# Kernel tuning notes

Hardware: AMD Instinct MI355X
Metric: run time of the kernel (lower is better)

Reference implementation:

```python
import jax, jax.numpy as jnp
import numpy as np

EPS = 1e-08


def setup_inputs() -> dict:
    key = jax.random.key(0)
    k1, k2 = jax.random.split(key)
    n, d = 8192, 64
    x = jax.random.normal(k1, (n, d), dtype=jnp.float32)
    y = jax.random.randint(k2, (n,), 0, 10, dtype=jnp.int64)
    # weights = 1 / temperature_init = 1 / 0.1
    weights = jnp.full((1,), 10.0, dtype=jnp.float32)
    return {"x": x, "y": y, "weights": weights}


def reference(x, y, weights):
    n = x.shape[0]
    # pairwise euclidean distances (torch.cdist p=2)
    sq = jnp.sum(x * x, axis=1)                      # [n]
    d2 = sq[:, None] + sq[None, :] - 2.0 * (x @ x.T)  # [n,n]
    eye = jnp.eye(n, dtype=bool)
    d2 = jnp.maximum(d2, 0.0)
    dist = jnp.where(eye, 0.0, jnp.sqrt(jnp.where(eye, 1.0, d2)))  # safe sqrt on diag
    expo = jnp.exp(-dist * weights[0])               # [n,n]
    same = (y[:, None] == y[None, :]) & ~eye         # same-class, excluding self
    top = jnp.sum(jnp.where(same, expo, 0.0), axis=1)  # [n]
    bot = jnp.sum(jnp.where(~eye, expo, 0.0), axis=1)  # [n]
    fracs = jnp.log(top / (bot + EPS))
    loss = -jnp.mean(fracs)
    return loss
```

## Files before the change

### kernel.cpp

```cpp
#include <hip/hip_runtime.h>

typedef _Float16 f16x8 __attribute__((ext_vector_type(8)));
typedef float    f32x4 __attribute__((ext_vector_type(4)));
typedef float    f32x2 __attribute__((ext_vector_type(2)));

#define N_ROWS 8192
#define DIM 64
#define EPS 1e-8f
#define LOG2E 1.4426950408889634f
#define SHIFT 64.0f
#define SHIFT_LN 44.361419555836499802f
#define TILE_I 256
#define NBI (N_ROWS / TILE_I)
#define TB 512
#define MAXC 17


__global__ void snn_prep(const float* __restrict__ x, _Float16* __restrict__ xh,
                         _Float16* __restrict__ xl, float* __restrict__ sq,
                         float* __restrict__ top, float* __restrict__ bot,
                         float* __restrict__ out) {
    const int gt = blockIdx.x * 256 + threadIdx.x;
    if (gt < N_ROWS) { top[gt] = 0.0f; bot[gt] = 0.0f; }
    if (gt == 0) out[0] = 0.0f;
    const int row = gt >> 6, lane = threadIdx.x & 63;
    float v = x[row * DIM + lane];
    _Float16 h = (_Float16)v;
    _Float16 l = (_Float16)(v - (float)h);
    xh[row * DIM + lane] = h;
    xl[row * DIM + lane] = l;
    float s = v * v;
    #pragma unroll
    for (int off = 32; off > 0; off >>= 1) s += __shfl_xor(s, off, 64);
    if (lane == 0) sq[row] = s;
}

__global__ __launch_bounds__(256, 2) void snn_mfma(
    const _Float16* __restrict__ xh, const _Float16* __restrict__ xl,
    const float* __restrict__ sq, const int* __restrict__ y,
    const float* __restrict__ w,
    float* __restrict__ top, float* __restrict__ bot)
{
    __shared__ float s_sqj[MAXC * 16];
    __shared__ int   s_yj[MAXC * 16];
    __shared__ f32x2 s_j[4][4][MAXC * 16];

    const int bid = blockIdx.x;
    int bi = 0, kk = 0, cum = 0;
    for (int p = 0; p < NBI; p++) {
        int nb = (p < 16) ? p + 1 : p;
        if (bid < cum + nb) { bi = p; kk = bid - cum; break; }
        cum += nb;
    }
    int c0, len;
    if (bi < 16)      { c0 = 16 * kk;              len = 16; }
    else if (kk < 16) { c0 = 17 * kk;              len = 17; }
    else              { c0 = 272 + 16 * (kk - 16); len = 16; }
    const int ndch = min(max(16 * bi - c0, 0), len);
    const int I0 = bi * TILE_I;

    const int tid = threadIdx.x, wv = tid >> 6, lane = tid & 63;
    const int mrow = lane & 15, kq = lane >> 4;

    for (int t = tid; t < len * 16; t += 256) {
        s_sqj[t] = sq[c0 * 16 + t];
        s_yj[t]  = y[c0 * 16 + t];
    }
    __syncthreads();

    const int iw = I0 + wv * 64;

    f16x8 ah[4][2], al[4][2];
    #pragma unroll
    for (int mt = 0; mt < 4; mt++)
        #pragma unroll
        for (int kc = 0; kc < 2; kc++) {
            int a = (iw + mt * 16 + mrow) * DIM + kc * 32 + kq * 8;
            ah[mt][kc] = *(const f16x8*)(xh + a);
            al[mt][kc] = *(const f16x8*)(xl + a);
        }

    float sqi[4][4]; int ypack[4];
    #pragma unroll
    for (int mt = 0; mt < 4; mt++) {
        int yp = 0;
        #pragma unroll
        for (int rr = 0; rr < 4; rr++) {
            int i = iw + mt * 16 + kq * 4 + rr;
            sqi[mt][rr] = sq[i];
            yp |= (y[i] & 255) << (8 * rr);
        }
        ypack[mt] = yp;
    }

    float ts[4][4], bs[4][4];
    #pragma unroll
    for (int mt = 0; mt < 4; mt++)
        #pragma unroll
        for (int rr = 0; rr < 4; rr++) { ts[mt][rr] = 0.0f; bs[mt][rr] = 0.0f; }

    const float c1 = -w[0] * LOG2E;
    f32x4 acc[4];

#define DECL_LOAD(N, NTL)                                                        \
    const int jr##N = (c0 + (NTL)) * 16 + mrow;                                  \
    const int boff##N = jr##N * DIM + kq * 8;                                    \
    f16x8 cbh0##N = *(const f16x8*)(xh + boff##N);                               \
    f16x8 cbh1##N = *(const f16x8*)(xh + boff##N + 32);                          \
    f16x8 cbl0##N = *(const f16x8*)(xl + boff##N);                               \
    f16x8 cbl1##N = *(const f16x8*)(xl + boff##N + 32);                          \
    const float sqj##N = s_sqj[(NTL) * 16 + mrow];                               \
    const int   yj##N  = s_yj[(NTL) * 16 + mrow];

#define DO_MFMA(N)                                                               \
    _Pragma("unroll")                                                            \
    for (int mt = 0; mt < 4; mt++) acc[mt] = (f32x4){0.f, 0.f, 0.f, 0.f};        \
    _Pragma("unroll")                                                            \
    for (int mt = 0; mt < 4; mt++)                                               \
        acc[mt] = __builtin_amdgcn_mfma_f32_16x16x32_f16(ah[mt][0], cbh0##N, acc[mt], 0, 0, 0); \
    _Pragma("unroll")                                                            \
    for (int mt = 0; mt < 4; mt++)                                               \
        acc[mt] = __builtin_amdgcn_mfma_f32_16x16x32_f16(ah[mt][1], cbh1##N, acc[mt], 0, 0, 0); \
    _Pragma("unroll")                                                            \
    for (int mt = 0; mt < 4; mt++)                                               \
        acc[mt] = __builtin_amdgcn_mfma_f32_16x16x32_f16(ah[mt][0], cbl0##N, acc[mt], 0, 0, 0); \
    _Pragma("unroll")                                                            \
    for (int mt = 0; mt < 4; mt++)                                               \
        acc[mt] = __builtin_amdgcn_mfma_f32_16x16x32_f16(ah[mt][1], cbl1##N, acc[mt], 0, 0, 0); \
    _Pragma("unroll")                                                            \
    for (int mt = 0; mt < 4; mt++)                                               \
        acc[mt] = __builtin_amdgcn_mfma_f32_16x16x32_f16(al[mt][0], cbh0##N, acc[mt], 0, 0, 0); \
    _Pragma("unroll")                                                            \
    for (int mt = 0; mt < 4; mt++)                                               \
        acc[mt] = __builtin_amdgcn_mfma_f32_16x16x32_f16(al[mt][1], cbh1##N, acc[mt], 0, 0, 0);

#define EPI_BOTH(N, NTL)                                                         \
    {                                                                            \
        float jt = 0.0f, jb = 0.0f;                                              \
        _Pragma("unroll")                                                        \
        for (int mt = 0; mt < 4; mt++)                                           \
            _Pragma("unroll")                                                    \
            for (int rr = 0; rr < 4; rr++) {                                     \
                float d2 = fmaf(-2.0f, acc[mt][rr], sqi[mt][rr] + sqj##N);       \
                d2 = fmaxf(d2, 0.0f);                                            \
                float dist = __builtin_amdgcn_sqrtf(d2);                         \
                float e2 = __builtin_amdgcn_exp2f(fmaf(c1, dist, SHIFT));        \
                float e2t = (yj##N == ((ypack[mt] >> (8 * rr)) & 255)) ? e2 : 0.0f; \
                ts[mt][rr] += e2t;                                               \
                bs[mt][rr] += e2;                                                \
                jt += e2t;                                                       \
                jb += e2;                                                        \
            }                                                                    \
        s_j[wv][kq][(NTL) * 16 + mrow] = (f32x2){jt, jb};       \
    }

#define EPI_DIAG(N, NTL)                                                         \
    {                                                                            \
        _Pragma("unroll")                                                        \
        for (int mt = 0; mt < 4; mt++)                                           \
            _Pragma("unroll")                                                    \
            for (int rr = 0; rr < 4; rr++) {                                     \
                int i = iw + mt * 16 + kq * 4 + rr;                              \
                float d2 = fmaf(-2.0f, acc[mt][rr], sqi[mt][rr] + sqj##N);       \
                d2 = fmaxf(d2, 0.0f);                                            \
                float dist = __builtin_amdgcn_sqrtf(d2);                         \
                float e2 = __builtin_amdgcn_exp2f(fmaf(c1, dist, SHIFT));        \
                bool offd = (i != jr##N);                                        \
                bool same = offd && (yj##N == ((ypack[mt] >> (8 * rr)) & 255));  \
                bs[mt][rr] += offd ? e2 : 0.0f;                                  \
                ts[mt][rr] += same ? e2 : 0.0f;                                  \
            }                                                                    \
    }

    int ntl = 0;
    for (; ntl + 2 <= ndch; ntl += 2) {
        DECL_LOAD(0, ntl)
        DECL_LOAD(1, ntl + 1)
        DO_MFMA(0) EPI_BOTH(0, ntl)
        DO_MFMA(1) EPI_BOTH(1, ntl + 1)
    }
    for (; ntl < ndch; ntl++) {
        DECL_LOAD(0, ntl)
        DO_MFMA(0) EPI_BOTH(0, ntl)
    }
    for (; ntl + 2 <= len; ntl += 2) {
        DECL_LOAD(0, ntl)
        DECL_LOAD(1, ntl + 1)
        DO_MFMA(0) EPI_DIAG(0, ntl)
        DO_MFMA(1) EPI_DIAG(1, ntl + 1)
    }
    for (; ntl < len; ntl++) {
        DECL_LOAD(0, ntl)
        DO_MFMA(0) EPI_DIAG(0, ntl)
    }
#undef DECL_LOAD
#undef DO_MFMA
#undef EPI_BOTH
#undef EPI_DIAG

    #pragma unroll
    for (int mt = 0; mt < 4; mt++)
        #pragma unroll
        for (int rr = 0; rr < 4; rr++) {
            float tv = ts[mt][rr], bv = bs[mt][rr];
            #pragma unroll
            for (int off = 1; off < 16; off <<= 1) {
                tv += __shfl_xor(tv, off, 64);
                bv += __shfl_xor(bv, off, 64);
            }
            if (mrow == 0) {
                int i = iw + mt * 16 + kq * 4 + rr;
                atomicAdd(&top[i], tv);
                atomicAdd(&bot[i], bv);
            }
        }

    if (ndch > 0) {
        __syncthreads();
        for (int t = tid; t < ndch * 16; t += 256) {
            float tt = 0.0f, bb = 0.0f;
            #pragma unroll
            for (int v = 0; v < 4; v++)
                #pragma unroll
                for (int q = 0; q < 4; q++) {
                    f32x2 s = s_j[v][q][t];
                    tt += s[0];
                    bb += s[1];
                }
            atomicAdd(&top[c0 * 16 + t], tt);
            atomicAdd(&bot[c0 * 16 + t], bb);
        }
    }
}

__global__ __launch_bounds__(256) void snn_final(
    const float* __restrict__ top, const float* __restrict__ bot,
    float* __restrict__ out)
{
    const int i = blockIdx.x * 256 + threadIdx.x;
    float t = top[i];
    float b = bot[i] * 0x1p-64f + EPS;
    float acc = (logf(t) - SHIFT_LN) - logf(b);
    #pragma unroll
    for (int off = 32; off > 0; off >>= 1) acc += __shfl_xor(acc, off, 64);
    __shared__ float red[4];
    if ((threadIdx.x & 63) == 0) red[threadIdx.x >> 6] = acc;
    __syncthreads();
    if (threadIdx.x == 0) {
        float s = red[0] + red[1] + red[2] + red[3];
        atomicAdd(out, -s / (float)N_ROWS);
    }
}

extern "C" void kernel_launch(void* const* d_in, const int* in_sizes, int n_in,
                              void* d_out, int out_size, void* d_ws, size_t ws_size,
                              hipStream_t stream) {
    const float* x = (const float*)d_in[0];
    const int*   y = (const int*)d_in[1];
    const float* w = (const float*)d_in[2];
    float* out = (float*)d_out;

    float* ws  = (float*)d_ws;
    float* top = ws;
    float* bot = ws + N_ROWS;
    float* sq  = ws + 2 * N_ROWS;
    _Float16* xh = (_Float16*)(ws + 3 * N_ROWS);
    _Float16* xl = xh + (size_t)N_ROWS * DIM;

    snn_prep<<<N_ROWS / 4, 256, 0, stream>>>(x, xh, xl, sq, top, bot, out);
    snn_mfma<<<TB, 256, 0, stream>>>(xh, xl, sq, y, w, top, bot);
    snn_final<<<N_ROWS / 256, 256, 0, stream>>>(top, bot, out);
}
```

Baseline: 94.26 us.

## Fuse final reduction into main kernel via last-block counter; vectorize prep

The separate final log/mean kernel is removed. Its work now runs in the last block of the MFMA kernel, found with a global atomic counter plus a thread fence. The prep kernel handles two floats per thread with half the blocks. This saves one kernel launch and its gap, but the final reduction now runs serially in a single block at the tail, and correctness depends on the counter reset in prep.

```diff
diff --git a/kernel.cpp b/kernel.cpp
--- a/kernel.cpp
+++ b/kernel.cpp
@@ -1,6 +1,7 @@
 #include <hip/hip_runtime.h>
 
 typedef _Float16 f16x8 __attribute__((ext_vector_type(8)));
+typedef _Float16 f16x2 __attribute__((ext_vector_type(2)));
 typedef float    f32x4 __attribute__((ext_vector_type(4)));
 typedef float    f32x2 __attribute__((ext_vector_type(2)));
 
@@ -15,6 +16,8 @@
 #define TB 512
 #define MAXC 17
 
+__device__ unsigned int g_ctr;
+
 
 __global__ void snn_prep(const float* __restrict__ x, _Float16* __restrict__ xh,
                          _Float16* __restrict__ xl, float* __restrict__ sq,
@@ -22,28 +25,34 @@
                          float* __restrict__ out) {
     const int gt = blockIdx.x * 256 + threadIdx.x;
     if (gt < N_ROWS) { top[gt] = 0.0f; bot[gt] = 0.0f; }
-    if (gt == 0) out[0] = 0.0f;
-    const int row = gt >> 6, lane = threadIdx.x & 63;
-    float v = x[row * DIM + lane];
-    _Float16 h = (_Float16)v;
-    _Float16 l = (_Float16)(v - (float)h);
-    xh[row * DIM + lane] = h;
-    xl[row * DIM + lane] = l;
-    float s = v * v;
-    #pragma unroll
-    for (int off = 32; off > 0; off >>= 1) s += __shfl_xor(s, off, 64);
-    if (lane == 0) sq[row] = s;
+    if (gt == 0) { out[0] = 0.0f; g_ctr = 0u; }
+    const int lane = threadIdx.x & 63;
+    const int row = gt >> 5;
+    const int cp  = (lane & 31) * 2;
+    f32x2 v = *(const f32x2*)(x + row * DIM + cp);
+    _Float16 h0 = (_Float16)v[0], h1 = (_Float16)v[1];
+    _Float16 l0 = (_Float16)(v[0] - (float)h0);
+    _Float16 l1 = (_Float16)(v[1] - (float)h1);
+    *(f16x2*)(xh + row * DIM + cp) = (f16x2){h0, h1};
+    *(f16x2*)(xl + row * DIM + cp) = (f16x2){l0, l1};
+    float s = v[0] * v[0] + v[1] * v[1];
+    #pragma unroll
+    for (int off = 16; off > 0; off >>= 1) s += __shfl_xor(s, off, 64);
+    if ((lane & 31) == 0) sq[row] = s;
 }
 
 __global__ __launch_bounds__(256, 2) void snn_mfma(
     const _Float16* __restrict__ xh, const _Float16* __restrict__ xl,
     const float* __restrict__ sq, const int* __restrict__ y,
     const float* __restrict__ w,
-    float* __restrict__ top, float* __restrict__ bot)
+    float* __restrict__ top, float* __restrict__ bot,
+    float* __restrict__ out)
 {
     __shared__ float s_sqj[MAXC * 16];
     __shared__ int   s_yj[MAXC * 16];
     __shared__ f32x2 s_j[4][4][MAXC * 16];
+    __shared__ bool  s_last;
+    __shared__ float s_red[4];
 
     const int bid = blockIdx.x;
     int bi = 0, kk = 0, cum = 0;
@@ -231,24 +240,24 @@
             atomicAdd(&bot[c0 * 16 + t], bb);
         }
     }
-}
-
-__global__ __launch_bounds__(256) void snn_final(
-    const float* __restrict__ top, const float* __restrict__ bot,
-    float* __restrict__ out)
-{
-    const int i = blockIdx.x * 256 + threadIdx.x;
-    float t = top[i];
-    float b = bot[i] * 0x1p-64f + EPS;
-    float acc = (logf(t) - SHIFT_LN) - logf(b);
-    #pragma unroll
-    for (int off = 32; off > 0; off >>= 1) acc += __shfl_xor(acc, off, 64);
-    __shared__ float red[4];
-    if ((threadIdx.x & 63) == 0) red[threadIdx.x >> 6] = acc;
+
+    __threadfence();
     __syncthreads();
-    if (threadIdx.x == 0) {
-        float s = red[0] + red[1] + red[2] + red[3];
-        atomicAdd(out, -s / (float)N_ROWS);
+    if (tid == 0) s_last = (atomicAdd(&g_ctr, 1u) == TB - 1);
+    __syncthreads();
+    if (s_last) {
+        float acc2 = 0.0f;
+        for (int r2 = tid; r2 < N_ROWS; r2 += 256) {
+            float t = __hip_atomic_load(&top[r2], __ATOMIC_RELAXED, __HIP_MEMORY_SCOPE_AGENT);
+            float b = __hip_atomic_load(&bot[r2], __ATOMIC_RELAXED, __HIP_MEMORY_SCOPE_AGENT);
+            acc2 += (logf(t) - SHIFT_LN) - logf(b * 0x1p-64f + EPS);
+        }
+        #pragma unroll
+        for (int off = 32; off > 0; off >>= 1) acc2 += __shfl_xor(acc2, off, 64);
+        if ((tid & 63) == 0) s_red[tid >> 6] = acc2;
+        __syncthreads();
+        if (tid == 0)
+            out[0] = -(s_red[0] + s_red[1] + s_red[2] + s_red[3]) / (float)N_ROWS;
     }
 }
 
@@ -267,7 +276,6 @@
     _Float16* xh = (_Float16*)(ws + 3 * N_ROWS);
     _Float16* xl = xh + (size_t)N_ROWS * DIM;
 
-    snn_prep<<<N_ROWS / 4, 256, 0, stream>>>(x, xh, xl, sq, top, bot, out);
-    snn_mfma<<<TB, 256, 0, stream>>>(xh, xl, sq, y, w, top, bot);
-    snn_final<<<N_ROWS / 256, 256, 0, stream>>>(top, bot, out);
+    snn_prep<<<N_ROWS / 8, 256, 0, stream>>>(x, xh, xl, sq, top, bot, out);
+    snn_mfma<<<TB, 256, 0, stream>>>(xh, xl, sq, y, w, top, bot, out);
 }
```

Result: slower. 125.0 us (+32.6%).
